# Kernel tuning notes

Hardware: AMD Instinct MI355X
Metric: run time of the kernel (lower is better)

## Reference

```python
import jax, jax.numpy as jnp
import numpy as np

B, K, LQ, LR, H = 32, 8, 128, 256, 512  # H = hidden_dim*2
L = LQ + K * LR


def setup_inputs() -> dict:
    key = jax.random.key(0)
    ks = jax.random.split(key, 10)
    w = 0.02
    return {
        "h_q": jax.random.normal(ks[0], (B, LQ, H), jnp.float32),
        "q_mask": jnp.ones((B, LQ), jnp.float32),
        "h_r": jax.random.normal(ks[1], (B, K, LR, H), jnp.float32),
        "r_mask": jnp.ones((B, K, LR), jnp.float32),
        "s_t": jax.random.normal(ks[2], (B, H), jnp.float32),
        "qr_cov": jnp.zeros((B, L), jnp.float32),
        # Linear weights stored torch-style [out, in]
        "U_w": jax.random.normal(ks[3], (H, H), jnp.float32) * w,
        "Wc_w": jax.random.normal(ks[4], (H, 1), jnp.float32) * w,
        "Ws_w": jax.random.normal(ks[5], (H, H), jnp.float32) * w,
        "Wqr_w": jax.random.normal(ks[6], (H, H), jnp.float32) * w,
        "Wqr_b": jax.random.normal(ks[7], (H,), jnp.float32) * w,
        "Vr_w": jax.random.normal(ks[8], (1, H), jnp.float32) * w,
    }


def reference(h_q, q_mask, h_r, r_mask, s_t, qr_cov,
              U_w, Wc_w, Ws_w, Wqr_w, Wqr_b, Vr_w):
    b, l_q, h = h_q.shape
    _, k, l_r, _ = h_r.shape

    _h_q = jnp.broadcast_to(h_q[:, None], (b, k, l_q, h)).reshape(b * k, l_q, h)
    _h_r = h_r.reshape(b * k, l_r, h)
    _q_mask = jnp.broadcast_to(q_mask[:, None], (b, k, l_q)).reshape(b * k, l_q)
    _r_mask = r_mask.reshape(b * k, l_r)

    # bilinear co-attention scores: tanh((hq @ U^T) @ hr^T)  [b*k, l_q, l_r]
    hqU = jnp.einsum('bqi,oi->bqo', _h_q, U_w)
    U = jnp.tanh(jnp.einsum('bqo,bro->bqr', hqU, _h_r))

    alpha_q = jax.nn.softmax(jnp.max(U, axis=2), axis=-1)  # [b*k, l_q]
    alpha_r = jax.nn.softmax(jnp.max(U, axis=1), axis=-1)  # [b*k, l_r]

    pai_q = ((alpha_q * _q_mask)[..., None] * _h_q).reshape(b, k, l_q, h).mean(axis=1)
    pai_r = ((alpha_r * _r_mask)[..., None] * _h_r).reshape(b, k * l_r, h)
    qr = jnp.concatenate([pai_q, pai_r], axis=1)  # [b, L, h]

    dec_fea = (jnp.einsum('bi,oi->bo', s_t, Ws_w)[:, None, :]
               + jnp.einsum('bli,oi->blo', qr, Wqr_w) + Wqr_b
               + qr_cov[:, :, None] * Wc_w[:, 0])  # coverage feature

    logits = jnp.einsum('blo,o->bl', jnp.tanh(dec_fea), Vr_w[0])  # [b, L]
    mask = jnp.concatenate([q_mask, r_mask.reshape(b, k * l_r)], axis=1)
    a = jax.nn.softmax(logits, axis=1) * mask
    a = a / jnp.sum(a, axis=1, keepdims=True)

    c_t = jnp.einsum('bl,blh->bh', a, qr)
    new_cov = qr_cov + a
    return (c_t, a, new_cov)
```

## Files before the change

### kernel.cpp

```cpp
#include <hip/hip_runtime.h>
#include <stdint.h>

#define B  32
#define KK 8
#define LQ 128
#define LR 256
#define H  512
#define LL 2176
#define STRIDE 40

typedef short s16x8 __attribute__((ext_vector_type(8)));
typedef float f32x4 __attribute__((ext_vector_type(4)));

__device__ __forceinline__ unsigned short f2bf(float f) {
    unsigned int u = __float_as_uint(f);
    unsigned int r = (u + 0x7FFFu + ((u >> 16) & 1u)) >> 16;
    return (unsigned short)r;
}
__device__ __forceinline__ float bf2f(unsigned short h) {
    return __uint_as_float(((unsigned int)h) << 16);
}
__device__ __forceinline__ void gload16(const unsigned short* g, unsigned short* l) {
    __builtin_amdgcn_global_load_lds(
        (const __attribute__((address_space(1))) void*)g,
        (__attribute__((address_space(3))) void*)l, 16, 0, 0);
}

#define NCONV (B * LL + 2 * H)
#define NZERO 168
__global__ __launch_bounds__(128) void k0_convert(
    const float* __restrict__ h_q, const float* __restrict__ h_r,
    const float* __restrict__ U_w, const float* __restrict__ Wqr_w,
    unsigned short* __restrict__ Xb, unsigned short* __restrict__ Uwb,
    unsigned short* __restrict__ Wqrb, float* __restrict__ logits,
    float* __restrict__ out) {
    int blk = blockIdx.x;
    int t = threadIdx.x;
    if (blk >= NCONV) {
        int base = (blk - NCONV) * 512 + t * 4;
        float4 z = {0.f, 0.f, 0.f, 0.f};
        if (base < B * LL) *(float4*)(logits + base) = z;
        else *(float4*)(out + base - B * LL) = z;
        return;
    }
    const float* src; unsigned short* dst;
    if (blk < B * LL) {
        int b = blk / LL, l = blk % LL;
        src = (l < LQ) ? (h_q + (size_t)(b * LQ + l) * H)
                       : (h_r + (size_t)(b * (KK * LR) + (l - LQ)) * H);
        dst = Xb + (size_t)blk * H;
    } else if (blk < B * LL + H) {
        int i = blk - B * LL;
        src = U_w + (size_t)i * H; dst = Uwb + (size_t)i * H;
    } else {
        int i = blk - B * LL - H;
        src = Wqr_w + (size_t)i * H; dst = Wqrb + (size_t)i * H;
    }
    float4 v = *(const float4*)(src + t * 4);
    ushort4 o;
    o.x = f2bf(v.x); o.y = f2bf(v.y); o.z = f2bf(v.z); o.w = f2bf(v.w);
    *(ushort4*)(dst + t * 4) = o;
}

__global__ __launch_bounds__(256) void k1_gemm_hqU(
    const unsigned short* __restrict__ Xb, const unsigned short* __restrict__ Uwb,
    unsigned short* __restrict__ hqU) {
    __shared__ __align__(16) unsigned short As[64 * STRIDE];
    __shared__ __align__(16) unsigned short Bs[64 * STRIDE];
    int tid = threadIdx.x;
    int wave = tid >> 6, lane = tid & 63;
    int quad = lane >> 4, l16 = lane & 15;
    int wr = wave >> 1, wc = wave & 1;
    int m0 = blockIdx.x * 64, n0 = blockIdx.y * 64;

    f32x4 acc[2][2] = {};
    int srow = tid >> 2, sk8 = tid & 3;
    int am = m0 + srow;
    size_t arow = (size_t)(am >> 7) * LL + (am & 127);
    for (int k0 = 0; k0 < H; k0 += 32) {
        *(uint4*)&As[srow * STRIDE + sk8 * 8] =
            *(const uint4*)(Xb + arow * H + k0 + sk8 * 8);
        *(uint4*)&Bs[srow * STRIDE + sk8 * 8] =
            *(const uint4*)(Uwb + (size_t)(n0 + srow) * H + k0 + sk8 * 8);
        __syncthreads();
        s16x8 af[2], bfr[2];
#pragma unroll
        for (int mi = 0; mi < 2; ++mi)
            af[mi] = *(const s16x8*)&As[(wr * 32 + mi * 16 + l16) * STRIDE + quad * 8];
#pragma unroll
        for (int ni = 0; ni < 2; ++ni)
            bfr[ni] = *(const s16x8*)&Bs[(wc * 32 + ni * 16 + l16) * STRIDE + quad * 8];
#pragma unroll
        for (int mi = 0; mi < 2; ++mi)
#pragma unroll
            for (int ni = 0; ni < 2; ++ni)
                acc[mi][ni] = __builtin_amdgcn_mfma_f32_16x16x32_bf16(
                    af[mi], bfr[ni], acc[mi][ni], 0, 0, 0);
        __syncthreads();
    }
#pragma unroll
    for (int mi = 0; mi < 2; ++mi)
#pragma unroll
        for (int ni = 0; ni < 2; ++ni)
#pragma unroll
            for (int i = 0; i < 4; ++i) {
                int row = m0 + wr * 32 + mi * 16 + quad * 4 + i;
                int col = n0 + wc * 32 + ni * 16 + l16;
                hqU[(size_t)row * H + col] = f2bf(acc[mi][ni][i]);
            }
}

__global__ __launch_bounds__(256) void k2_scores(
    const unsigned short* __restrict__ hqU, const unsigned short* __restrict__ Xb,
    float* __restrict__ maxq_part, float* __restrict__ maxr_part) {
    __shared__ __align__(16) unsigned short As[64 * 64];
    __shared__ __align__(16) unsigned short Bs[128 * 64];
    __shared__ float redA[64 * 2];
    __shared__ float redB[128 * 2];
    int idx = blockIdx.x;
    int rt = idx & 1, qt = (idx >> 1) & 1, k = (idx >> 2) & 7, b = idx >> 5;
    int tid = threadIdx.x;
    int wave = tid >> 6, lane = tid & 63;
    int quad = lane >> 4, l16 = lane & 15;
    int wr = wave >> 1, wc = wave & 1;

    const unsigned short* Ab = hqU + (size_t)(b * LQ + qt * 64) * H;
    const unsigned short* Bb = Xb + (size_t)(b * LL + LQ + k * LR + rt * 128) * H;

    const unsigned short* ag[2]; unsigned short* la[2];
    const unsigned short* bg[4]; unsigned short* lb[4];
#pragma unroll
    for (int i = 0; i < 2; ++i) {
        int g = (wave * 2 + i) * 64 + lane;
        int r = g >> 3, c = g & 7, cs = c ^ (r & 7);
        ag[i] = Ab + (size_t)r * H + cs * 8;
        la[i] = As + (wave * 2 + i) * 512;
    }
#pragma unroll
    for (int i = 0; i < 4; ++i) {
        int g = (wave * 4 + i) * 64 + lane;
        int r = g >> 3, c = g & 7, cs = c ^ (r & 7);
        bg[i] = Bb + (size_t)r * H + cs * 8;
        lb[i] = Bs + (wave * 4 + i) * 512;
    }

    f32x4 acc[2][4] = {};
    for (int k0 = 0; k0 < H; k0 += 64) {
#pragma unroll
        for (int i = 0; i < 2; ++i) gload16(ag[i] + k0, la[i]);
#pragma unroll
        for (int i = 0; i < 4; ++i) gload16(bg[i] + k0, lb[i]);
        __syncthreads();
#pragma unroll
        for (int kh = 0; kh < 2; ++kh) {
            s16x8 af[2], bfr[4];
#pragma unroll
            for (int mi = 0; mi < 2; ++mi) {
                int row = wr * 32 + mi * 16 + l16;
                int ch = (kh * 4 + quad) ^ (row & 7);
                af[mi] = *(const s16x8*)&As[(row * 8 + ch) * 8];
            }
#pragma unroll
            for (int ni = 0; ni < 4; ++ni) {
                int row = wc * 64 + ni * 16 + l16;
                int ch = (kh * 4 + quad) ^ (row & 7);
                bfr[ni] = *(const s16x8*)&Bs[(row * 8 + ch) * 8];
            }
#pragma unroll
            for (int mi = 0; mi < 2; ++mi)
#pragma unroll
                for (int ni = 0; ni < 4; ++ni)
                    acc[mi][ni] = __builtin_amdgcn_mfma_f32_16x16x32_bf16(
                        af[mi], bfr[ni], acc[mi][ni], 0, 0, 0);
        }
        __syncthreads();
    }
#pragma unroll
    for (int mi = 0; mi < 2; ++mi)
#pragma unroll
        for (int i = 0; i < 4; ++i) {
            float v = acc[mi][0][i];
            v = fmaxf(v, acc[mi][1][i]);
            v = fmaxf(v, acc[mi][2][i]);
            v = fmaxf(v, acc[mi][3][i]);
            for (int s = 1; s < 16; s <<= 1) v = fmaxf(v, __shfl_xor(v, s));
            if (l16 == 0) redA[(wr * 32 + mi * 16 + quad * 4 + i) * 2 + wc] = v;
        }
#pragma unroll
    for (int ni = 0; ni < 4; ++ni) {
        float v = acc[0][ni][0];
#pragma unroll
        for (int mi = 0; mi < 2; ++mi)
#pragma unroll
            for (int i = 0; i < 4; ++i) v = fmaxf(v, acc[mi][ni][i]);
        for (int s = 16; s < 64; s <<= 1) v = fmaxf(v, __shfl_xor(v, s));
        if (quad == 0) redB[(wc * 64 + ni * 16 + l16) * 2 + wr] = v;
    }
    __syncthreads();
    size_t base = (size_t)(b * KK + k);
    if (tid < 64) {
        float v = fmaxf(redA[tid * 2 + 0], redA[tid * 2 + 1]);
        maxq_part[(base * 2 + rt) * 128 + qt * 64 + tid] = v;
    }
    if (tid < 128) {
        float v = fmaxf(redB[tid * 2 + 0], redB[tid * 2 + 1]);
        maxr_part[(base * 2 + qt) * 256 + rt * 128 + tid] = v;
    }
}

__global__ __launch_bounds__(256) void k3a_alphas(
    const float* __restrict__ maxq_part, const float* __restrict__ maxr_part,
    const float* __restrict__ r_mask, float* __restrict__ alpha_q,
    float* __restrict__ wbuf) {
    int b = blockIdx.x >> 3, k = blockIdx.x & 7;
    int t = threadIdx.x;
    __shared__ float red[256];
    size_t base = (size_t)(b * KK + k);
    float vq = -1e30f;
    if (t < 128)
        vq = tanhf(fmaxf(maxq_part[(base * 2 + 0) * 128 + t],
                         maxq_part[(base * 2 + 1) * 128 + t]));
    red[t] = vq; __syncthreads();
    for (int s = 128; s > 0; s >>= 1) { if (t < s) red[t] = fmaxf(red[t], red[t + s]); __syncthreads(); }
    float mxq = red[0]; __syncthreads();
    float eq = (t < 128) ? expf(vq - mxq) : 0.f;
    red[t] = eq; __syncthreads();
    for (int s = 128; s > 0; s >>= 1) { if (t < s) red[t] += red[t + s]; __syncthreads(); }
    float invq = 1.f / red[0]; __syncthreads();
    if (t < 128) alpha_q[base * 128 + t] = eq * invq;
    float vr = tanhf(fmaxf(maxr_part[(base * 2 + 0) * 256 + t],
                           maxr_part[(base * 2 + 1) * 256 + t]));
    red[t] = vr; __syncthreads();
    for (int s = 128; s > 0; s >>= 1) { if (t < s) red[t] = fmaxf(red[t], red[t + s]); __syncthreads(); }
    float mxr = red[0]; __syncthreads();
    float er = expf(vr - mxr);
    red[t] = er; __syncthreads();
    for (int s = 128; s > 0; s >>= 1) { if (t < s) red[t] += red[t + s]; __syncthreads(); }
    float invr = 1.f / red[0];
    wbuf[b * LL + LQ + k * LR + t] = r_mask[base * LR + t] * er * invr;
}

__global__ __launch_bounds__(256) void k3b_sws(
    const float* __restrict__ alpha_q, const float* __restrict__ q_mask,
    const float* __restrict__ s_t, const float* __restrict__ Ws_w,
    float* __restrict__ wbuf, float* __restrict__ sWs) {
    int b = blockIdx.x, oc = blockIdx.y;
    int t = threadIdx.x;
    __shared__ __align__(16) float sl[H];
    for (int i = t; i < H; i += 256) sl[i] = s_t[b * H + i];
    __syncthreads();
    if (oc == 0 && t < 128) {
        float s = 0.f;
#pragma unroll
        for (int k = 0; k < KK; ++k) s += alpha_q[(size_t)(b * KK + k) * 128 + t];
        wbuf[b * LL + t] = q_mask[b * LQ + t] * s * 0.125f;
    }
    int o = oc * 64 + (t >> 2);
    int part = t & 3;
    const float4* sl4 = (const float4*)sl;
    const float4* wr4 = (const float4*)(Ws_w + (size_t)o * H);
    float a = 0.f;
    for (int i = part * 32; i < part * 32 + 32; ++i) {
        float4 x = sl4[i], y = wr4[i];
        a += x.x * y.x + x.y * y.y + x.z * y.z + x.w * y.w;
    }
    a += __shfl_xor(a, 1);
    a += __shfl_xor(a, 2);
    if (part == 0) sWs[b * H + o] = a;
}

__global__ __launch_bounds__(256) void k4_gemm_logits(
    const unsigned short* __restrict__ Xb, const unsigned short* __restrict__ Wqrb,
    const float* __restrict__ sWs, const float* __restrict__ Wqr_b,
    const float* __restrict__ Wc_w, const float* __restrict__ Vr_w,
    const float* __restrict__ wbuf, const float* __restrict__ qr_cov,
    float* __restrict__ logits) {
    __shared__ __align__(16) unsigned short As[128 * 64];
    __shared__ __align__(16) unsigned short Bs[128 * 64];
    __shared__ float wrow[128], covrow[128], sWsl[128], biasl[128], wcl[128], vrl[128];
    int tid = threadIdx.x;
    int wave = tid >> 6, lane = tid & 63;
    int quad = lane >> 4, l16 = lane & 15;
    int wr = wave >> 1, wc = wave & 1;
    size_t m0 = (size_t)blockIdx.x * 128;
    int n0 = blockIdx.y * 128;
    int b = (int)(m0 / LL);
    int l0 = (int)(m0 % LL);

    const unsigned short* ag[4]; unsigned short* la[4];
    const unsigned short* bg[4]; unsigned short* lb[4];
#pragma unroll
    for (int i = 0; i < 4; ++i) {
        int g = (wave * 4 + i) * 64 + lane;
        int r = g >> 3, c = g & 7, cs = c ^ (r & 7);
        ag[i] = Xb + (m0 + r) * H + cs * 8;
        bg[i] = Wqrb + (size_t)(n0 + r) * H + cs * 8;
        la[i] = As + (wave * 4 + i) * 512;
        lb[i] = Bs + (wave * 4 + i) * 512;
    }

    f32x4 acc[4][4] = {};
    for (int k0 = 0; k0 < H; k0 += 64) {
#pragma unroll
        for (int i = 0; i < 4; ++i) gload16(ag[i] + k0, la[i]);
#pragma unroll
        for (int i = 0; i < 4; ++i) gload16(bg[i] + k0, lb[i]);
        __syncthreads();
#pragma unroll
        for (int kh = 0; kh < 2; ++kh) {
            s16x8 af[4], bfr[4];
#pragma unroll
            for (int mi = 0; mi < 4; ++mi) {
                int row = wr * 64 + mi * 16 + l16;
                int ch = (kh * 4 + quad) ^ (row & 7);
                af[mi] = *(const s16x8*)&As[(row * 8 + ch) * 8];
            }
#pragma unroll
            for (int ni = 0; ni < 4; ++ni) {
                int row = wc * 64 + ni * 16 + l16;
                int ch = (kh * 4 + quad) ^ (row & 7);
                bfr[ni] = *(const s16x8*)&Bs[(row * 8 + ch) * 8];
            }
#pragma unroll
            for (int mi = 0; mi < 4; ++mi)
#pragma unroll
                for (int ni = 0; ni < 4; ++ni)
                    acc[mi][ni] = __builtin_amdgcn_mfma_f32_16x16x32_bf16(
                        af[mi], bfr[ni], acc[mi][ni], 0, 0, 0);
        }
        __syncthreads();
    }
    if (tid < 128) {
        wrow[tid]   = wbuf[b * LL + l0 + tid];
        covrow[tid] = qr_cov[b * LL + l0 + tid];
        sWsl[tid]   = sWs[b * H + n0 + tid];
        biasl[tid]  = Wqr_b[n0 + tid];
        wcl[tid]    = Wc_w[n0 + tid];
        vrl[tid]    = Vr_w[n0 + tid];
    }
    __syncthreads();
#pragma unroll
    for (int mi = 0; mi < 4; ++mi)
#pragma unroll
        for (int i = 0; i < 4; ++i) {
            int rl = wr * 64 + mi * 16 + quad * 4 + i;
            float wv = wrow[rl], cv = covrow[rl];
            float lsum = 0.f;
#pragma unroll
            for (int ni = 0; ni < 4; ++ni) {
                int ol = wc * 64 + ni * 16 + l16;
                float dec = sWsl[ol] + wv * acc[mi][ni][i] + biasl[ol] + cv * wcl[ol];
                lsum += vrl[ol] * tanhf(dec);
            }
            for (int s = 1; s < 16; s <<= 1) lsum += __shfl_xor(lsum, s);
            if (l16 == 0) atomicAdd(&logits[b * LL + l0 + rl], lsum);
        }
}

__global__ __launch_bounds__(256) void k5a_softmax(
    const float* __restrict__ logits, const float* __restrict__ q_mask,
    const float* __restrict__ r_mask, const float* __restrict__ qr_cov,
    const float* __restrict__ wbuf, float* __restrict__ out,
    float* __restrict__ coef) {
    int b = blockIdx.x, t = threadIdx.x;
    __shared__ float red[256];
    float mx = -1e30f;
    for (int l = t; l < LL; l += 256) mx = fmaxf(mx, logits[b * LL + l]);
    red[t] = mx; __syncthreads();
    for (int s = 128; s > 0; s >>= 1) { if (t < s) red[t] = fmaxf(red[t], red[t + s]); __syncthreads(); }
    mx = red[0]; __syncthreads();
    float sum = 0.f;
    for (int l = t; l < LL; l += 256) {
        float e = expf(logits[b * LL + l] - mx);
        float m = (l < LQ) ? q_mask[b * LQ + l] : r_mask[b * (KK * LR) + l - LQ];
        sum += e * m;
    }
    red[t] = sum; __syncthreads();
    for (int s = 128; s > 0; s >>= 1) { if (t < s) red[t] += red[t + s]; __syncthreads(); }
    float inv = 1.f / red[0];
    float* aout = out + B * H + (size_t)b * LL;
    float* cov  = out + B * H + (size_t)B * LL + (size_t)b * LL;
    for (int l = t; l < LL; l += 256) {
        float e = expf(logits[b * LL + l] - mx);
        float m = (l < LQ) ? q_mask[b * LQ + l] : r_mask[b * (KK * LR) + l - LQ];
        float a = e * m * inv;
        aout[l] = a;
        cov[l] = qr_cov[b * LL + l] + a;
        coef[b * LL + l] = a * wbuf[b * LL + l];
    }
}

__global__ __launch_bounds__(256) void k5b_ct(
    const unsigned short* __restrict__ Xb, const float* __restrict__ coef,
    float* __restrict__ out) {
    int b = blockIdx.x / 17, chunk = blockIdx.x % 17;
    int t = threadIdx.x;
    int l0 = chunk * 128;
    __shared__ float cl[128];
    if (t < 128) cl[t] = coef[b * LL + l0 + t];
    __syncthreads();
    int rr = t >> 7;
    int cc = (t & 127) * 4;
    float a0 = 0.f, a1 = 0.f, a2 = 0.f, a3 = 0.f;
    const unsigned short* xp = Xb + ((size_t)b * LL + l0) * H;
    for (int l = 0; l < 128; l += 2) {
        float c = cl[l + rr];
        ushort4 u = *(const ushort4*)(xp + (size_t)(l + rr) * H + cc);
        a0 += c * bf2f(u.x);
        a1 += c * bf2f(u.y);
        a2 += c * bf2f(u.z);
        a3 += c * bf2f(u.w);
    }
    atomicAdd(&out[b * H + cc + 0], a0);
    atomicAdd(&out[b * H + cc + 1], a1);
    atomicAdd(&out[b * H + cc + 2], a2);
    atomicAdd(&out[b * H + cc + 3], a3);
}

extern "C" void kernel_launch(void* const* d_in, const int* in_sizes, int n_in,
                              void* d_out, int out_size, void* d_ws, size_t ws_size,
                              hipStream_t stream) {
    (void)in_sizes; (void)n_in; (void)out_size; (void)ws_size;
    const float* h_q    = (const float*)d_in[0];
    const float* q_mask = (const float*)d_in[1];
    const float* h_r    = (const float*)d_in[2];
    const float* r_mask = (const float*)d_in[3];
    const float* s_t    = (const float*)d_in[4];
    const float* qr_cov = (const float*)d_in[5];
    const float* U_w    = (const float*)d_in[6];
    const float* Wc_w   = (const float*)d_in[7];
    const float* Ws_w   = (const float*)d_in[8];
    const float* Wqr_w  = (const float*)d_in[9];
    const float* Wqr_b  = (const float*)d_in[10];
    const float* Vr_w   = (const float*)d_in[11];
    float* out = (float*)d_out;

    char* p = (char*)d_ws;
    unsigned short* Xb   = (unsigned short*)p; p += (size_t)B * LL * H * 2;
    unsigned short* Uwb  = (unsigned short*)p; p += (size_t)H * H * 2;
    unsigned short* Wqrb = (unsigned short*)p; p += (size_t)H * H * 2;
    unsigned short* hqU  = (unsigned short*)p; p += (size_t)B * LQ * H * 2;
    float* sWs       = (float*)p; p += (size_t)B * H * 4;
    float* maxq_part = (float*)p; p += (size_t)B * KK * 2 * 128 * 4;
    float* maxr_part = (float*)p; p += (size_t)B * KK * 2 * 256 * 4;
    float* alpha_q   = (float*)p; p += (size_t)B * KK * 128 * 4;
    float* wbuf      = (float*)p; p += (size_t)B * LL * 4;
    float* logits    = (float*)p; p += (size_t)B * LL * 4;
    float* coef      = (float*)p; p += (size_t)B * LL * 4;

    k0_convert<<<NCONV + NZERO, 128, 0, stream>>>(h_q, h_r, U_w, Wqr_w, Xb, Uwb, Wqrb,
                                                  logits, out);
    k1_gemm_hqU<<<dim3((B * LQ) / 64, H / 64), 256, 0, stream>>>(Xb, Uwb, hqU);
    k2_scores<<<B * KK * 4, 256, 0, stream>>>(hqU, Xb, maxq_part, maxr_part);
    k3a_alphas<<<B * KK, 256, 0, stream>>>(maxq_part, maxr_part, r_mask, alpha_q, wbuf);
    k3b_sws<<<dim3(B, 8), 256, 0, stream>>>(alpha_q, q_mask, s_t, Ws_w, wbuf, sWs);
    k4_gemm_logits<<<dim3((B * LL) / 128, H / 128), 256, 0, stream>>>(
        Xb, Wqrb, sWs, Wqr_b, Wc_w, Vr_w, wbuf, qr_cov, logits);
    k5a_softmax<<<B, 256, 0, stream>>>(logits, q_mask, r_mask, qr_cov, wbuf, out, coef);
    k5b_ct<<<B * (LL / 128), 256, 0, stream>>>(Xb, coef, out);
}
```

Baseline: 388.6 us.

## Tune conversion, fast tanh/exp, k4 tile swizzle, softmax caching, wider ct reduction

The conversion kernel becomes a grid-stride loop with contiguous float4 chunks instead of one block per row. tanh and exp in the alpha, logits-epilogue and softmax kernels switch to exp2/rcp intrinsics. The logits GEMM remaps block indices so the four N tiles of an M tile and neighbouring M tiles run on nearby blocks, improving L2 reuse, and its epilogue parameter loads move before the main loop. The softmax caches logits and masked exponentials in LDS to avoid a second global read and exp, and the context kernel uses 16-byte loads with an LDS reduction that halves the atomics. Fast tanh and exp add small approximation error.

```diff
diff --git a/kernel.cpp b/kernel.cpp
--- a/kernel.cpp
+++ b/kernel.cpp
@@ -25,41 +25,72 @@
         (const __attribute__((address_space(1))) void*)g,
         (__attribute__((address_space(3))) void*)l, 16, 0, 0);
 }
-
-#define NCONV (B * LL + 2 * H)
-#define NZERO 168
-__global__ __launch_bounds__(128) void k0_convert(
+__device__ __forceinline__ float fexp2(float x) {
+#if __has_builtin(__builtin_amdgcn_exp2f)
+    return __builtin_amdgcn_exp2f(x);
+#else
+    return __expf(x * 0.69314718056f);
+#endif
+}
+__device__ __forceinline__ float frcp(float x) {
+#if __has_builtin(__builtin_amdgcn_rcpf)
+    return __builtin_amdgcn_rcpf(x);
+#else
+    return 1.f / x;
+#endif
+}
+__device__ __forceinline__ float fast_tanh(float x) {
+    float e = fexp2(x * 2.885390082f);
+    return 1.f - 2.f * frcp(1.f + e);
+}
+#define LOG2E 1.4426950408889634f
+
+#define NQ4 (B * LQ * H / 4)
+#define NR4 (B * KK * LR * H / 4)
+#define NW4 (H * H / 4)
+#define NL4 (B * LL / 4)
+#define NC4 (B * H / 4)
+#define NTOT4 (NQ4 + NR4 + 2 * NW4 + NL4 + NC4)
+__global__ __launch_bounds__(256) void k0_convert(
     const float* __restrict__ h_q, const float* __restrict__ h_r,
     const float* __restrict__ U_w, const float* __restrict__ Wqr_w,
     unsigned short* __restrict__ Xb, unsigned short* __restrict__ Uwb,
     unsigned short* __restrict__ Wqrb, float* __restrict__ logits,
-    float* __restrict__ out) {
-    int blk = blockIdx.x;
-    int t = threadIdx.x;
-    if (blk >= NCONV) {
-        int base = (blk - NCONV) * 512 + t * 4;
-        float4 z = {0.f, 0.f, 0.f, 0.f};
-        if (base < B * LL) *(float4*)(logits + base) = z;
-        else *(float4*)(out + base - B * LL) = z;
-        return;
-    }
-    const float* src; unsigned short* dst;
-    if (blk < B * LL) {
-        int b = blk / LL, l = blk % LL;
-        src = (l < LQ) ? (h_q + (size_t)(b * LQ + l) * H)
-                       : (h_r + (size_t)(b * (KK * LR) + (l - LQ)) * H);
-        dst = Xb + (size_t)blk * H;
-    } else if (blk < B * LL + H) {
-        int i = blk - B * LL;
-        src = U_w + (size_t)i * H; dst = Uwb + (size_t)i * H;
-    } else {
-        int i = blk - B * LL - H;
-        src = Wqr_w + (size_t)i * H; dst = Wqrb + (size_t)i * H;
-    }
-    float4 v = *(const float4*)(src + t * 4);
-    ushort4 o;
-    o.x = f2bf(v.x); o.y = f2bf(v.y); o.z = f2bf(v.z); o.w = f2bf(v.w);
-    *(ushort4*)(dst + t * 4) = o;
+    float* __restrict__ out_ct) {
+    for (unsigned int u = blockIdx.x * 256 + threadIdx.x; u < NTOT4;
+         u += gridDim.x * 256) {
+        if (u < NQ4 + NR4) {
+            const float* src; unsigned short* dst;
+            if (u < NQ4) {
+                unsigned int f = u * 4;
+                unsigned int b = f >> 16, rem = f & 65535u;
+                src = h_q + f;
+                dst = Xb + (size_t)b * (LL * H) + rem;
+            } else {
+                unsigned int f = (u - NQ4) * 4;
+                unsigned int b = f >> 20, rem = f & 1048575u;
+                src = h_r + f;
+                dst = Xb + (size_t)b * (LL * H) + LQ * H + rem;
+            }
+            float4 v = *(const float4*)src;
+            ushort4 o;
+            o.x = f2bf(v.x); o.y = f2bf(v.y); o.z = f2bf(v.z); o.w = f2bf(v.w);
+            *(ushort4*)dst = o;
+        } else if (u < NQ4 + NR4 + 2 * NW4) {
+            unsigned int v4 = u - (NQ4 + NR4);
+            const float* src = (v4 < NW4) ? (U_w + v4 * 4) : (Wqr_w + (v4 - NW4) * 4);
+            unsigned short* dst = (v4 < NW4) ? (Uwb + v4 * 4) : (Wqrb + (v4 - NW4) * 4);
+            float4 v = *(const float4*)src;
+            ushort4 o;
+            o.x = f2bf(v.x); o.y = f2bf(v.y); o.z = f2bf(v.z); o.w = f2bf(v.w);
+            *(ushort4*)dst = o;
+        } else {
+            unsigned int z = u - (NQ4 + NR4 + 2 * NW4);
+            float4 zero = {0.f, 0.f, 0.f, 0.f};
+            if (z < NL4) *(float4*)(logits + z * 4) = zero;
+            else *(float4*)(out_ct + (z - NL4) * 4) = zero;
+        }
+    }
 }
 
 __global__ __launch_bounds__(256) void k1_gemm_hqU(
@@ -218,22 +249,22 @@
     size_t base = (size_t)(b * KK + k);
     float vq = -1e30f;
     if (t < 128)
-        vq = tanhf(fmaxf(maxq_part[(base * 2 + 0) * 128 + t],
-                         maxq_part[(base * 2 + 1) * 128 + t]));
+        vq = fast_tanh(fmaxf(maxq_part[(base * 2 + 0) * 128 + t],
+                             maxq_part[(base * 2 + 1) * 128 + t]));
     red[t] = vq; __syncthreads();
     for (int s = 128; s > 0; s >>= 1) { if (t < s) red[t] = fmaxf(red[t], red[t + s]); __syncthreads(); }
     float mxq = red[0]; __syncthreads();
-    float eq = (t < 128) ? expf(vq - mxq) : 0.f;
+    float eq = (t < 128) ? fexp2((vq - mxq) * LOG2E) : 0.f;
     red[t] = eq; __syncthreads();
     for (int s = 128; s > 0; s >>= 1) { if (t < s) red[t] += red[t + s]; __syncthreads(); }
     float invq = 1.f / red[0]; __syncthreads();
     if (t < 128) alpha_q[base * 128 + t] = eq * invq;
-    float vr = tanhf(fmaxf(maxr_part[(base * 2 + 0) * 256 + t],
-                           maxr_part[(base * 2 + 1) * 256 + t]));
+    float vr = fast_tanh(fmaxf(maxr_part[(base * 2 + 0) * 256 + t],
+                               maxr_part[(base * 2 + 1) * 256 + t]));
     red[t] = vr; __syncthreads();
     for (int s = 128; s > 0; s >>= 1) { if (t < s) red[t] = fmaxf(red[t], red[t + s]); __syncthreads(); }
     float mxr = red[0]; __syncthreads();
-    float er = expf(vr - mxr);
+    float er = fexp2((vr - mxr) * LOG2E);
     red[t] = er; __syncthreads();
     for (int s = 128; s > 0; s >>= 1) { if (t < s) red[t] += red[t + s]; __syncthreads(); }
     float invr = 1.f / red[0];
@@ -282,54 +313,14 @@
     int wave = tid >> 6, lane = tid & 63;
     int quad = lane >> 4, l16 = lane & 15;
     int wr = wave >> 1, wc = wave & 1;
-    size_t m0 = (size_t)blockIdx.x * 128;
-    int n0 = blockIdx.y * 128;
+    int g = blockIdx.x;
+    int tle = (g & 7) * 272 + (g >> 3);
+    int mt = tle >> 2, nt = tle & 3;
+    size_t m0 = (size_t)mt * 128;
+    int n0 = nt * 128;
     int b = (int)(m0 / LL);
     int l0 = (int)(m0 % LL);
 
-    const unsigned short* ag[4]; unsigned short* la[4];
-    const unsigned short* bg[4]; unsigned short* lb[4];
-#pragma unroll
-    for (int i = 0; i < 4; ++i) {
-        int g = (wave * 4 + i) * 64 + lane;
-        int r = g >> 3, c = g & 7, cs = c ^ (r & 7);
-        ag[i] = Xb + (m0 + r) * H + cs * 8;
-        bg[i] = Wqrb + (size_t)(n0 + r) * H + cs * 8;
-        la[i] = As + (wave * 4 + i) * 512;
-        lb[i] = Bs + (wave * 4 + i) * 512;
-    }
-
-    f32x4 acc[4][4] = {};
-    for (int k0 = 0; k0 < H; k0 += 64) {
-#pragma unroll
-        for (int i = 0; i < 4; ++i) gload16(ag[i] + k0, la[i]);
-#pragma unroll
-        for (int i = 0; i < 4; ++i) gload16(bg[i] + k0, lb[i]);
-        __syncthreads();
-#pragma unroll
-        for (int kh = 0; kh < 2; ++kh) {
-            s16x8 af[4], bfr[4];
-#pragma unroll
-            for (int mi = 0; mi < 4; ++mi) {
-                int row = wr * 64 + mi * 16 + l16;
-                int ch = (kh * 4 + quad) ^ (row & 7);
-                af[mi] = *(const s16x8*)&As[(row * 8 + ch) * 8];
-            }
-#pragma unroll
-            for (int ni = 0; ni < 4; ++ni) {
-                int row = wc * 64 + ni * 16 + l16;
-                int ch = (kh * 4 + quad) ^ (row & 7);
-                bfr[ni] = *(const s16x8*)&Bs[(row * 8 + ch) * 8];
-            }
-#pragma unroll
-            for (int mi = 0; mi < 4; ++mi)
-#pragma unroll
-                for (int ni = 0; ni < 4; ++ni)
-                    acc[mi][ni] = __builtin_amdgcn_mfma_f32_16x16x32_bf16(
-                        af[mi], bfr[ni], acc[mi][ni], 0, 0, 0);
-        }
-        __syncthreads();
-    }
     if (tid < 128) {
         wrow[tid]   = wbuf[b * LL + l0 + tid];
         covrow[tid] = qr_cov[b * LL + l0 + tid];
@@ -338,7 +329,50 @@
         wcl[tid]    = Wc_w[n0 + tid];
         vrl[tid]    = Vr_w[n0 + tid];
     }
-    __syncthreads();
+
+    const unsigned short* ag[4]; unsigned short* la[4];
+    const unsigned short* bg[4]; unsigned short* lb[4];
+#pragma unroll
+    for (int i = 0; i < 4; ++i) {
+        int gg = (wave * 4 + i) * 64 + lane;
+        int r = gg >> 3, c = gg & 7, cs = c ^ (r & 7);
+        ag[i] = Xb + (m0 + r) * H + cs * 8;
+        bg[i] = Wqrb + (size_t)(n0 + r) * H + cs * 8;
+        la[i] = As + (wave * 4 + i) * 512;
+        lb[i] = Bs + (wave * 4 + i) * 512;
+    }
+
+    f32x4 acc[4][4] = {};
+    for (int k0 = 0; k0 < H; k0 += 64) {
+#pragma unroll
+        for (int i = 0; i < 4; ++i) gload16(ag[i] + k0, la[i]);
+#pragma unroll
+        for (int i = 0; i < 4; ++i) gload16(bg[i] + k0, lb[i]);
+        __syncthreads();
+#pragma unroll
+        for (int kh = 0; kh < 2; ++kh) {
+            s16x8 af[4], bfr[4];
+#pragma unroll
+            for (int mi = 0; mi < 4; ++mi) {
+                int row = wr * 64 + mi * 16 + l16;
+                int ch = (kh * 4 + quad) ^ (row & 7);
+                af[mi] = *(const s16x8*)&As[(row * 8 + ch) * 8];
+            }
+#pragma unroll
+            for (int ni = 0; ni < 4; ++ni) {
+                int row = wc * 64 + ni * 16 + l16;
+                int ch = (kh * 4 + quad) ^ (row & 7);
+                bfr[ni] = *(const s16x8*)&Bs[(row * 8 + ch) * 8];
+            }
+#pragma unroll
+            for (int mi = 0; mi < 4; ++mi)
+#pragma unroll
+                for (int ni = 0; ni < 4; ++ni)
+                    acc[mi][ni] = __builtin_amdgcn_mfma_f32_16x16x32_bf16(
+                        af[mi], bfr[ni], acc[mi][ni], 0, 0, 0);
+        }
+        __syncthreads();
+    }
 #pragma unroll
     for (int mi = 0; mi < 4; ++mi)
 #pragma unroll
@@ -350,7 +384,7 @@
             for (int ni = 0; ni < 4; ++ni) {
                 int ol = wc * 64 + ni * 16 + l16;
                 float dec = sWsl[ol] + wv * acc[mi][ni][i] + biasl[ol] + cv * wcl[ol];
-                lsum += vrl[ol] * tanhf(dec);
+                lsum += vrl[ol] * fast_tanh(dec);
             }
             for (int s = 1; s < 16; s <<= 1) lsum += __shfl_xor(lsum, s);
             if (l16 == 0) atomicAdd(&logits[b * LL + l0 + rl], lsum);
@@ -363,27 +397,33 @@
     const float* __restrict__ wbuf, float* __restrict__ out,
     float* __restrict__ coef) {
     int b = blockIdx.x, t = threadIdx.x;
+    __shared__ float lg[LL];
     __shared__ float red[256];
     float mx = -1e30f;
-    for (int l = t; l < LL; l += 256) mx = fmaxf(mx, logits[b * LL + l]);
+    for (int l = t; l < LL; l += 256) {
+        float v = logits[b * LL + l];
+        lg[l] = v;
+        mx = fmaxf(mx, v);
+    }
     red[t] = mx; __syncthreads();
     for (int s = 128; s > 0; s >>= 1) { if (t < s) red[t] = fmaxf(red[t], red[t + s]); __syncthreads(); }
     mx = red[0]; __syncthreads();
     float sum = 0.f;
     for (int l = t; l < LL; l += 256) {
-        float e = expf(logits[b * LL + l] - mx);
+        float e = fexp2((lg[l] - mx) * LOG2E);
         float m = (l < LQ) ? q_mask[b * LQ + l] : r_mask[b * (KK * LR) + l - LQ];
-        sum += e * m;
+        float em = e * m;
+        lg[l] = em;
+        sum += em;
     }
     red[t] = sum; __syncthreads();
     for (int s = 128; s > 0; s >>= 1) { if (t < s) red[t] += red[t + s]; __syncthreads(); }
     float inv = 1.f / red[0];
+    __syncthreads();
     float* aout = out + B * H + (size_t)b * LL;
     float* cov  = out + B * H + (size_t)B * LL + (size_t)b * LL;
     for (int l = t; l < LL; l += 256) {
-        float e = expf(logits[b * LL + l] - mx);
-        float m = (l < LQ) ? q_mask[b * LQ + l] : r_mask[b * (KK * LR) + l - LQ];
-        float a = e * m * inv;
+        float a = lg[l] * inv;
         aout[l] = a;
         cov[l] = qr_cov[b * LL + l] + a;
         coef[b * LL + l] = a * wbuf[b * LL + l];
@@ -397,24 +437,32 @@
     int t = threadIdx.x;
     int l0 = chunk * 128;
     __shared__ float cl[128];
+    __shared__ float red[4][512];
     if (t < 128) cl[t] = coef[b * LL + l0 + t];
     __syncthreads();
-    int rr = t >> 7;
-    int cc = (t & 127) * 4;
-    float a0 = 0.f, a1 = 0.f, a2 = 0.f, a3 = 0.f;
+    int rr = t >> 6, lane = t & 63, cc = lane * 8;
+    float a[8] = {};
     const unsigned short* xp = Xb + ((size_t)b * LL + l0) * H;
-    for (int l = 0; l < 128; l += 2) {
-        float c = cl[l + rr];
-        ushort4 u = *(const ushort4*)(xp + (size_t)(l + rr) * H + cc);
-        a0 += c * bf2f(u.x);
-        a1 += c * bf2f(u.y);
-        a2 += c * bf2f(u.z);
-        a3 += c * bf2f(u.w);
-    }
-    atomicAdd(&out[b * H + cc + 0], a0);
-    atomicAdd(&out[b * H + cc + 1], a1);
-    atomicAdd(&out[b * H + cc + 2], a2);
-    atomicAdd(&out[b * H + cc + 3], a3);
+    for (int l = rr; l < 128; l += 4) {
+        float c = cl[l];
+        uint4 u4 = *(const uint4*)(xp + (size_t)l * H + cc);
+        a[0] += c * __uint_as_float(u4.x << 16);
+        a[1] += c * __uint_as_float(u4.x & 0xffff0000u);
+        a[2] += c * __uint_as_float(u4.y << 16);
+        a[3] += c * __uint_as_float(u4.y & 0xffff0000u);
+        a[4] += c * __uint_as_float(u4.z << 16);
+        a[5] += c * __uint_as_float(u4.z & 0xffff0000u);
+        a[6] += c * __uint_as_float(u4.w << 16);
+        a[7] += c * __uint_as_float(u4.w & 0xffff0000u);
+    }
+#pragma unroll
+    for (int j = 0; j < 8; ++j) red[rr][cc + j] = a[j];
+    __syncthreads();
+    int col = t * 2;
+    float s0 = red[0][col] + red[1][col] + red[2][col] + red[3][col];
+    float s1 = red[0][col + 1] + red[1][col + 1] + red[2][col + 1] + red[3][col + 1];
+    atomicAdd(&out[b * H + col], s0);
+    atomicAdd(&out[b * H + col + 1], s1);
 }
 
 extern "C" void kernel_launch(void* const* d_in, const int* in_sizes, int n_in,
@@ -448,13 +496,13 @@
     float* logits    = (float*)p; p += (size_t)B * LL * 4;
     float* coef      = (float*)p; p += (size_t)B * LL * 4;
 
-    k0_convert<<<NCONV + NZERO, 128, 0, stream>>>(h_q, h_r, U_w, Wqr_w, Xb, Uwb, Wqrb,
-                                                  logits, out);
+    k0_convert<<<2048, 256, 0, stream>>>(h_q, h_r, U_w, Wqr_w, Xb, Uwb, Wqrb,
+                                         logits, out);
     k1_gemm_hqU<<<dim3((B * LQ) / 64, H / 64), 256, 0, stream>>>(Xb, Uwb, hqU);
     k2_scores<<<B * KK * 4, 256, 0, stream>>>(hqU, Xb, maxq_part, maxr_part);
     k3a_alphas<<<B * KK, 256, 0, stream>>>(maxq_part, maxr_part, r_mask, alpha_q, wbuf);
     k3b_sws<<<dim3(B, 8), 256, 0, stream>>>(alpha_q, q_mask, s_t, Ws_w, wbuf, sWs);
-    k4_gemm_logits<<<dim3((B * LL) / 128, H / 128), 256, 0, stream>>>(
+    k4_gemm_logits<<<2176, 256, 0, stream>>>(
         Xb, Wqrb, sWs, Wqr_b, Wc_w, Vr_w, wbuf, qr_cov, logits);
     k5a_softmax<<<B, 256, 0, stream>>>(logits, q_mask, r_mask, qr_cov, wbuf, out, coef);
     k5b_ct<<<B * (LL / 128), 256, 0, stream>>>(Xb, coef, out);
```

After: 360.2 us. -7.3%, faster.
